# Performance work log

Hardware: AMD Instinct MI355X
Metric: run time of the kernel (lower is better)

Reference implementation:

```python
import jax, jax.numpy as jnp
import numpy as np

DIM = 32    # hard-wired global `dim` in the source (== d_head)
OMEGA = 4   # hard-wired global `omega` (number of random features)


def setup_inputs() -> dict:
    key = jax.random.key(0)
    ks = jax.random.split(key, 8)
    B, T, E, D = 16, 4096, 1024, DIM  # n_embd=1024, n_head=32 -> d_head=32
    x = jax.random.normal(ks[0], (B, T, E), jnp.float32)
    # nn.Linear params, stored as [in, out] so y = x @ W + b
    wq = jax.random.normal(ks[1], (E, D), jnp.float32) * 0.02
    bq = jax.random.normal(ks[2], (D,), jnp.float32) * 0.02
    wk = jax.random.normal(ks[3], (E, D), jnp.float32) * 0.02
    bk = jax.random.normal(ks[4], (D,), jnp.float32) * 0.02
    wv = jax.random.normal(ks[5], (E, D), jnp.float32) * 0.02
    bv = jax.random.normal(ks[6], (D,), jnp.float32) * 0.02
    # random-feature matrix: torch.randn(omega, dim) materialized here
    # so the reference is deterministic
    w_raw = jax.random.normal(ks[7], (OMEGA, DIM), jnp.float32)
    return {"x": x, "wq": wq, "bq": bq, "wk": wk, "bk": bk,
            "wv": wv, "bv": bv, "w_raw": w_raw}


def reference(x, wq, bq, wk, bk, wv, bv, w_raw):
    # QKV projections (nn.Linear): [B,T,E] @ [E,D] -> [B,T,D]
    k = x @ wk + bk
    q = x @ wq + bq
    v = x @ wv + bv  # computed but never used, exactly as in the source
    del v
    # Aprox_softmax(k, q)
    w = w_raw.T                                      # [DIM, OMEGA]
    w = jnp.sqrt(jnp.asarray(DIM, x.dtype)) * (w / jnp.linalg.norm(w))
    k_norm = jnp.linalg.norm(k)                      # Frobenius norm (scalar)
    q_norm = jnp.linalg.norm(q)
    z = k + q                                        # [B,T,DIM]
    z_sqr = k_norm ** 2 + q_norm ** 2                # scalar
    lcosh = jnp.cosh(z @ w)                          # [B,T,OMEGA]
    a = jnp.exp(-z_sqr / 2)                          # scalar
    r = a * lcosh.mean(axis=-1)                      # [B,T]
    return r
```

## Files before the change

kernel.cpp:

```cpp
#include <hip/hip_runtime.h>
#include <math.h>


typedef float  floatx4 __attribute__((ext_vector_type(4)));
typedef float  f32x4   __attribute__((ext_vector_type(4)));
typedef int    intx4   __attribute__((ext_vector_type(4)));
typedef __bf16 bf16x8  __attribute__((ext_vector_type(8)));

union I4B8 { intx4 i; bf16x8 b; };

__device__ __forceinline__ unsigned pk2(float a, float b) {
    return (__builtin_bit_cast(unsigned, a) >> 16) |
           (__builtin_bit_cast(unsigned, b) & 0xffff0000u);
}

__global__ __launch_bounds__(256) void prep_btp_kernel(
    const float* __restrict__ wk, const float* __restrict__ wq,
    unsigned short* __restrict__ BtP)
{
    const int c = blockIdx.x * 256 + threadIdx.x;
    const int t    = c >> 9;
    const int sub  = (c >> 6) & 7;
    const int lane = c & 63;
    const int g  = sub >> 1, ks = sub & 1;
    const int lm = lane & 15, kg = lane >> 4;
    const int col = g * 16 + lm;
    const int kb  = t * 64 + ks * 32 + kg * 8;
    const float* src = (col < 32) ? (wk + col) : (wq + (col - 32));
    unsigned u[8];
    #pragma unroll
    for (int e = 0; e < 8; ++e)
        u[e] = __builtin_bit_cast(unsigned, src[(size_t)(kb + e) * 32]) >> 16;
    intx4 v;
    v.x = (int)(u[0] | (u[1] << 16));
    v.y = (int)(u[2] | (u[3] << 16));
    v.z = (int)(u[4] | (u[5] << 16));
    v.w = (int)(u[6] | (u[7] << 16));
    *(intx4*)(BtP + (size_t)c * 8) = v;
}

__global__ __launch_bounds__(256, 4) void head_mfma_kernel(
    const float* __restrict__ x,
    const unsigned short* __restrict__ BtP,
    const float* __restrict__ bq, const float* __restrict__ bk,
    const float* __restrict__ w_raw,
    float* __restrict__ out, float* __restrict__ partial)
{
    __shared__ char smem[25104];
    char*  As  = smem;
    char*  Bs  = smem + 8192;
    float* z_s = (float*)(smem + 8192);
    float* w_s = (float*)(smem + 24576);
    float* red = (float*)(smem + 25088);

    const int tid = threadIdx.x, lane = tid & 63, wv = tid >> 6;
    const int lm = lane & 15, kg = lane >> 4;
    const int row0 = blockIdx.x * 64;

    if (tid < 128) w_s[tid] = w_raw[tid];

    const float bias0 = bk[lm], bias1 = bk[16 + lm];
    const float bias2 = bq[lm], bias3 = bq[16 + lm];

    const int s_row = tid >> 3, s_kc = tid & 7;
    const int wr0 = ((s_row       * 128 + s_kc * 16) ^ ((s_row & 7) << 4));
    const int wr1 = (((s_row + 32) * 128 + s_kc * 16) ^ ((s_row & 7) << 4));
    const float* g0 = x + (size_t)(row0 + s_row) * 1024 + s_kc * 8;
    const float* g1 = g0 + 32 * 1024;

    const int fr_row = wv * 16 + lm;
    const int rd0 = ((fr_row * 128 + (kg)     * 16) ^ ((fr_row & 7) << 4));
    const int rd1 = ((fr_row * 128 + (4 + kg) * 16) ^ ((fr_row & 7) << 4));

    const unsigned short* bgp = BtP + (size_t)tid * 16;
    const int bwr = tid * 32;

    f32x4 acc[4] = {{0,0,0,0},{0,0,0,0},{0,0,0,0},{0,0,0,0}};
    floatx4 ra[2][4];
    intx4   rb[2][2];

    rb[0][0] = *(const intx4*)(bgp + 0);
    rb[0][1] = *(const intx4*)(bgp + 8);
    rb[1][0] = *(const intx4*)(bgp + 4096);
    rb[1][1] = *(const intx4*)(bgp + 4096 + 8);
    #pragma unroll
    for (int p = 0; p < 2; ++p) {
        ra[p][0] = *(const floatx4*)(g0 + p * 64);
        ra[p][1] = *(const floatx4*)(g0 + p * 64 + 4);
        ra[p][2] = *(const floatx4*)(g1 + p * 64);
        ra[p][3] = *(const floatx4*)(g1 + p * 64 + 4);
    }
    {
        intx4 w0, w1;
        w0.x = pk2(ra[0][0].x, ra[0][0].y); w0.y = pk2(ra[0][0].z, ra[0][0].w);
        w0.z = pk2(ra[0][1].x, ra[0][1].y); w0.w = pk2(ra[0][1].z, ra[0][1].w);
        w1.x = pk2(ra[0][2].x, ra[0][2].y); w1.y = pk2(ra[0][2].z, ra[0][2].w);
        w1.z = pk2(ra[0][3].x, ra[0][3].y); w1.w = pk2(ra[0][3].z, ra[0][3].w);
        *(intx4*)(As + wr0) = w0;
        *(intx4*)(As + wr1) = w1;
        *(intx4*)(Bs + bwr)      = rb[0][0];
        *(intx4*)(Bs + bwr + 16) = rb[0][1];
    }
    asm volatile("s_waitcnt lgkmcnt(0)" ::: "memory");
    __builtin_amdgcn_sched_barrier(0);
    __builtin_amdgcn_s_barrier();
    __builtin_amdgcn_sched_barrier(0);

    #pragma unroll
    for (int t = 0; t < 16; ++t) {
        const int cur = t & 1, nxt = (t + 1) & 1;

        if (t <= 13) {
            ra[cur][0] = *(const floatx4*)(g0 + (t + 2) * 64);
            ra[cur][1] = *(const floatx4*)(g0 + (t + 2) * 64 + 4);
            ra[cur][2] = *(const floatx4*)(g1 + (t + 2) * 64);
            ra[cur][3] = *(const floatx4*)(g1 + (t + 2) * 64 + 4);
        }
        {
            I4B8 a0; a0.i = *(intx4*)(As + rd0);
            I4B8 bf0[4];
            #pragma unroll
            for (int g = 0; g < 4; ++g)
                bf0[g].i = *(intx4*)(Bs + cur * 8192 + (g * 2) * 1024 + lane * 16);
            #pragma unroll
            for (int g = 0; g < 4; ++g)
                acc[g] = __builtin_amdgcn_mfma_f32_16x16x32_bf16(a0.b, bf0[g].b, acc[g], 0, 0, 0);
            I4B8 a1; a1.i = *(intx4*)(As + rd1);
            I4B8 bf1[4];
            #pragma unroll
            for (int g = 0; g < 4; ++g)
                bf1[g].i = *(intx4*)(Bs + cur * 8192 + (g * 2 + 1) * 1024 + lane * 16);
            #pragma unroll
            for (int g = 0; g < 4; ++g)
                acc[g] = __builtin_amdgcn_mfma_f32_16x16x32_bf16(a1.b, bf1[g].b, acc[g], 0, 0, 0);
        }
        __builtin_amdgcn_sched_barrier(0);
        __builtin_amdgcn_s_barrier();
        __builtin_amdgcn_sched_barrier(0);

        if (t <= 14) {
            intx4 w0, w1;
            w0.x = pk2(ra[nxt][0].x, ra[nxt][0].y); w0.y = pk2(ra[nxt][0].z, ra[nxt][0].w);
            w0.z = pk2(ra[nxt][1].x, ra[nxt][1].y); w0.w = pk2(ra[nxt][1].z, ra[nxt][1].w);
            w1.x = pk2(ra[nxt][2].x, ra[nxt][2].y); w1.y = pk2(ra[nxt][2].z, ra[nxt][2].w);
            w1.z = pk2(ra[nxt][3].x, ra[nxt][3].y); w1.w = pk2(ra[nxt][3].z, ra[nxt][3].w);
            *(intx4*)(As + wr0) = w0;
            *(intx4*)(As + wr1) = w1;
            *(intx4*)(Bs + nxt * 8192 + bwr)      = rb[nxt][0];
            *(intx4*)(Bs + nxt * 8192 + bwr + 16) = rb[nxt][1];
            if (t <= 13) {
                rb[cur][0] = *(const intx4*)(bgp + (size_t)(t + 2) * 4096);
                rb[cur][1] = *(const intx4*)(bgp + (size_t)(t + 2) * 4096 + 8);
            }
            asm volatile("s_waitcnt lgkmcnt(0)" ::: "memory");
            __builtin_amdgcn_sched_barrier(0);
            __builtin_amdgcn_s_barrier();
            __builtin_amdgcn_sched_barrier(0);
        }
    }

    __syncthreads();

    float ss = 0.f;
    const int rbase = wv * 16 + kg * 4;
    #pragma unroll
    for (int reg = 0; reg < 4; ++reg) {
        const float k0v = acc[0][reg] + bias0;
        const float k1v = acc[1][reg] + bias1;
        const float q0v = acc[2][reg] + bias2;
        const float q1v = acc[3][reg] + bias3;
        ss += k0v * k0v + k1v * k1v + q0v * q0v + q1v * q1v;
        const int rr = rbase + reg;
        z_s[rr * 33 + lm]      = k0v + q0v;
        z_s[rr * 33 + 16 + lm] = k1v + q1v;
    }

    #pragma unroll
    for (int off = 32; off > 0; off >>= 1) ss += __shfl_down(ss, off);
    if (lane == 0) red[wv] = ss;
    __syncthreads();
    if (tid == 0) partial[blockIdx.x] = red[0] + red[1] + red[2] + red[3];

    float wn = 0.f;
    #pragma unroll
    for (int i = 0; i < 128; ++i) wn += w_s[i] * w_s[i];
    const float scale = sqrtf(32.0f) / sqrtf(wn);

    const int r = tid >> 2;
    const int o = tid & 3;
    float t2 = 0.f;
    #pragma unroll
    for (int d = 0; d < 32; ++d)
        t2 += z_s[r * 33 + d] * w_s[o * 32 + d];
    t2 *= scale;
    float ch = coshf(t2);
    ch += __shfl_xor(ch, 1, 4);
    ch += __shfl_xor(ch, 2, 4);
    if (o == 0) out[row0 + r] = 0.25f * ch;
}

__global__ __launch_bounds__(256) void head_finalize_kernel(
    const float* __restrict__ partial, float* __restrict__ out)
{
    __shared__ float red[4];
    const int tid = threadIdx.x;
    float s = partial[tid] + partial[tid + 256] + partial[tid + 512] + partial[tid + 768];
    #pragma unroll
    for (int off = 32; off > 0; off >>= 1) s += __shfl_down(s, off);
    if ((tid & 63) == 0) red[tid >> 6] = s;
    __syncthreads();
    const float tot = red[0] + red[1] + red[2] + red[3];
    const float a = expf(-0.5f * tot);
    out[blockIdx.x * 256 + tid] *= a;
}

extern "C" void kernel_launch(void* const* d_in, const int* in_sizes, int n_in,
                              void* d_out, int out_size, void* d_ws, size_t ws_size,
                              hipStream_t stream) {
    (void)in_sizes; (void)n_in; (void)out_size; (void)ws_size;
    const float* x     = (const float*)d_in[0];
    const float* wq    = (const float*)d_in[1];
    const float* bq    = (const float*)d_in[2];
    const float* wk    = (const float*)d_in[3];
    const float* bk    = (const float*)d_in[4];
    const float* w_raw = (const float*)d_in[7];
    float* out = (float*)d_out;

    float*          partial = (float*)d_ws;
    unsigned short* BtP     = (unsigned short*)((char*)d_ws + 4096);

    prep_btp_kernel<<<32, 256, 0, stream>>>(wk, wq, BtP);
    head_mfma_kernel<<<1024, 256, 0, stream>>>(x, BtP, bq, bk, w_raw, out, partial);
    head_finalize_kernel<<<256, 256, 0, stream>>>(partial, out);
}
```

Measured before the change: 51.24 us.

## Single-buffer register prefetch, use hardware bf16 convert, raise occupancy to five

Replaces the two-deep register prefetch arrays for the x and B tiles with one set of registers, issuing the next global loads right after the current registers are written to shared memory. This cuts register pressure so launch bounds can move from 4 to 5 waves per SIMD. It also switches the truncating bf16 pack to a compiler bf16 conversion, which rounds differently and may cost more instructions. The trade-off is a shorter prefetch distance, so less global-load latency is hidden per wave, in exchange for more resident waves.

```diff
diff --git a/kernel.cpp b/kernel.cpp
--- a/kernel.cpp
+++ b/kernel.cpp
@@ -8,11 +8,6 @@
 typedef __bf16 bf16x8  __attribute__((ext_vector_type(8)));
 
 union I4B8 { intx4 i; bf16x8 b; };
-
-__device__ __forceinline__ unsigned pk2(float a, float b) {
-    return (__builtin_bit_cast(unsigned, a) >> 16) |
-           (__builtin_bit_cast(unsigned, b) & 0xffff0000u);
-}
 
 __global__ __launch_bounds__(256) void prep_btp_kernel(
     const float* __restrict__ wk, const float* __restrict__ wq,
@@ -39,7 +34,16 @@
     *(intx4*)(BtP + (size_t)c * 8) = v;
 }
 
-__global__ __launch_bounds__(256, 4) void head_mfma_kernel(
+__device__ __forceinline__ intx4 packA(floatx4 a, floatx4 b) {
+    I4B8 h;
+    h.b[0] = (__bf16)a.x; h.b[1] = (__bf16)a.y;
+    h.b[2] = (__bf16)a.z; h.b[3] = (__bf16)a.w;
+    h.b[4] = (__bf16)b.x; h.b[5] = (__bf16)b.y;
+    h.b[6] = (__bf16)b.z; h.b[7] = (__bf16)b.w;
+    return h.i;
+}
+
+__global__ __launch_bounds__(256, 5) void head_mfma_kernel(
     const float* __restrict__ x,
     const unsigned short* __restrict__ BtP,
     const float* __restrict__ bq, const float* __restrict__ bk,
@@ -63,7 +67,7 @@
     const float bias2 = bq[lm], bias3 = bq[16 + lm];
 
     const int s_row = tid >> 3, s_kc = tid & 7;
-    const int wr0 = ((s_row       * 128 + s_kc * 16) ^ ((s_row & 7) << 4));
+    const int wr0 = ((s_row        * 128 + s_kc * 16) ^ ((s_row & 7) << 4));
     const int wr1 = (((s_row + 32) * 128 + s_kc * 16) ^ ((s_row & 7) << 4));
     const float* g0 = x + (size_t)(row0 + s_row) * 1024 + s_kc * 8;
     const float* g1 = g0 + 32 * 1024;
@@ -76,31 +80,25 @@
     const int bwr = tid * 32;
 
     f32x4 acc[4] = {{0,0,0,0},{0,0,0,0},{0,0,0,0},{0,0,0,0}};
-    floatx4 ra[2][4];
-    intx4   rb[2][2];
-
-    rb[0][0] = *(const intx4*)(bgp + 0);
-    rb[0][1] = *(const intx4*)(bgp + 8);
-    rb[1][0] = *(const intx4*)(bgp + 4096);
-    rb[1][1] = *(const intx4*)(bgp + 4096 + 8);
-    #pragma unroll
-    for (int p = 0; p < 2; ++p) {
-        ra[p][0] = *(const floatx4*)(g0 + p * 64);
-        ra[p][1] = *(const floatx4*)(g0 + p * 64 + 4);
-        ra[p][2] = *(const floatx4*)(g1 + p * 64);
-        ra[p][3] = *(const floatx4*)(g1 + p * 64 + 4);
-    }
-    {
-        intx4 w0, w1;
-        w0.x = pk2(ra[0][0].x, ra[0][0].y); w0.y = pk2(ra[0][0].z, ra[0][0].w);
-        w0.z = pk2(ra[0][1].x, ra[0][1].y); w0.w = pk2(ra[0][1].z, ra[0][1].w);
-        w1.x = pk2(ra[0][2].x, ra[0][2].y); w1.y = pk2(ra[0][2].z, ra[0][2].w);
-        w1.z = pk2(ra[0][3].x, ra[0][3].y); w1.w = pk2(ra[0][3].z, ra[0][3].w);
-        *(intx4*)(As + wr0) = w0;
-        *(intx4*)(As + wr1) = w1;
-        *(intx4*)(Bs + bwr)      = rb[0][0];
-        *(intx4*)(Bs + bwr + 16) = rb[0][1];
-    }
+    floatx4 ra0, ra1, ra2, ra3;
+    intx4   rb0, rb1;
+
+    rb0 = *(const intx4*)(bgp);
+    rb1 = *(const intx4*)(bgp + 8);
+    ra0 = *(const floatx4*)(g0);
+    ra1 = *(const floatx4*)(g0 + 4);
+    ra2 = *(const floatx4*)(g1);
+    ra3 = *(const floatx4*)(g1 + 4);
+    *(intx4*)(As + wr0) = packA(ra0, ra1);
+    *(intx4*)(As + wr1) = packA(ra2, ra3);
+    *(intx4*)(Bs + bwr)      = rb0;
+    *(intx4*)(Bs + bwr + 16) = rb1;
+    ra0 = *(const floatx4*)(g0 + 64);
+    ra1 = *(const floatx4*)(g0 + 64 + 4);
+    ra2 = *(const floatx4*)(g1 + 64);
+    ra3 = *(const floatx4*)(g1 + 64 + 4);
+    rb0 = *(const intx4*)(bgp + 4096);
+    rb1 = *(const intx4*)(bgp + 4096 + 8);
     asm volatile("s_waitcnt lgkmcnt(0)" ::: "memory");
     __builtin_amdgcn_sched_barrier(0);
     __builtin_amdgcn_s_barrier();
@@ -110,12 +108,6 @@
     for (int t = 0; t < 16; ++t) {
         const int cur = t & 1, nxt = (t + 1) & 1;
 
-        if (t <= 13) {
-            ra[cur][0] = *(const floatx4*)(g0 + (t + 2) * 64);
-            ra[cur][1] = *(const floatx4*)(g0 + (t + 2) * 64 + 4);
-            ra[cur][2] = *(const floatx4*)(g1 + (t + 2) * 64);
-            ra[cur][3] = *(const floatx4*)(g1 + (t + 2) * 64 + 4);
-        }
         {
             I4B8 a0; a0.i = *(intx4*)(As + rd0);
             I4B8 bf0[4];
@@ -139,18 +131,17 @@
         __builtin_amdgcn_sched_barrier(0);
 
         if (t <= 14) {
-            intx4 w0, w1;
-            w0.x = pk2(ra[nxt][0].x, ra[nxt][0].y); w0.y = pk2(ra[nxt][0].z, ra[nxt][0].w);
-            w0.z = pk2(ra[nxt][1].x, ra[nxt][1].y); w0.w = pk2(ra[nxt][1].z, ra[nxt][1].w);
-            w1.x = pk2(ra[nxt][2].x, ra[nxt][2].y); w1.y = pk2(ra[nxt][2].z, ra[nxt][2].w);
-            w1.z = pk2(ra[nxt][3].x, ra[nxt][3].y); w1.w = pk2(ra[nxt][3].z, ra[nxt][3].w);
-            *(intx4*)(As + wr0) = w0;
-            *(intx4*)(As + wr1) = w1;
-            *(intx4*)(Bs + nxt * 8192 + bwr)      = rb[nxt][0];
-            *(intx4*)(Bs + nxt * 8192 + bwr + 16) = rb[nxt][1];
+            *(intx4*)(As + wr0) = packA(ra0, ra1);
+            *(intx4*)(As + wr1) = packA(ra2, ra3);
+            *(intx4*)(Bs + nxt * 8192 + bwr)      = rb0;
+            *(intx4*)(Bs + nxt * 8192 + bwr + 16) = rb1;
             if (t <= 13) {
-                rb[cur][0] = *(const intx4*)(bgp + (size_t)(t + 2) * 4096);
-                rb[cur][1] = *(const intx4*)(bgp + (size_t)(t + 2) * 4096 + 8);
+                ra0 = *(const floatx4*)(g0 + (t + 2) * 64);
+                ra1 = *(const floatx4*)(g0 + (t + 2) * 64 + 4);
+                ra2 = *(const floatx4*)(g1 + (t + 2) * 64);
+                ra3 = *(const floatx4*)(g1 + (t + 2) * 64 + 4);
+                rb0 = *(const intx4*)(bgp + (size_t)(t + 2) * 4096);
+                rb1 = *(const intx4*)(bgp + (size_t)(t + 2) * 4096 + 8);
             }
             asm volatile("s_waitcnt lgkmcnt(0)" ::: "memory");
             __builtin_amdgcn_sched_barrier(0);
```

After: 51.38 us. About the same (+0.3%).
